# Optimization experiments

Measured on AMD Instinct MI355X. Metric: run time of the kernel, lower is better.

## Reference

```python
import jax, jax.numpy as jnp
import numpy as np

B, N, C, K = 4, 1024, 384, 10


def _sqdist(a, b):
    # a: [B,P,3], b: [B,M,3] -> [B,P,M] squared euclidean distance
    d = (jnp.sum(a * a, -1)[:, :, None] + jnp.sum(b * b, -1)[:, None, :]
         - 2.0 * jnp.einsum('bpc,bmc->bpm', a, b))
    return jnp.maximum(d, 0.0)


def _gather(points, idx):
    # points: [B,M,C], idx: [B,...] int -> [B,...,C]  (index_points)
    return jax.vmap(lambda p, i: p[i])(points, idx)


def setup_inputs() -> dict:
    key = jax.random.key(0)
    ks = jax.random.split(key, 8)
    def lin(k_, fan_in, fan_out):
        return jax.random.normal(k_, (fan_in, fan_out), jnp.float32) * (1.0 / np.sqrt(fan_in))
    return {
        'q': jax.random.normal(ks[0], (B, N, C), jnp.float32),
        'q_pos': jax.random.normal(ks[1], (B, N, 3), jnp.float32),
        'Wv': lin(ks[2], C, C), 'bv': jnp.zeros((C,), jnp.float32),
        'W1': lin(ks[3], 2 * C, C), 'b1': jnp.zeros((C,), jnp.float32),
        'ln_g': jnp.ones((C,), jnp.float32), 'ln_b': jnp.zeros((C,), jnp.float32),
        'W2': lin(ks[4], C, 3),
        'Wk': lin(ks[5], 2 * C, C), 'bk': jnp.zeros((C,), jnp.float32),
    }


def reference(q, q_pos, Wv, bv, W1, b1, ln_g, ln_b, W2, Wk, bk):
    Bq, Nq, Cq = q.shape
    # 1) KNN of each query among all points (self-attn: v=q, v_pos=q_pos)
    d = _sqdist(q_pos, q_pos)                      # [B,N,N]
    _, idx = jax.lax.top_k(-d, K)                  # [B,N,K] (smallest distances)
    # 2) offset prediction from gathered projected features + query feature
    v_off = q @ Wv + bv                            # [B,N,C]
    off_local_v = _gather(v_off, idx)              # [B,N,K,C]
    qk = jnp.broadcast_to(q[:, :, None, :], (Bq, Nq, K, Cq))
    shift_feat = jnp.concatenate([off_local_v, qk], -1)  # [B,N,K,2C]
    h = shift_feat @ W1 + b1
    mu = jnp.mean(h, -1, keepdims=True)
    var = jnp.var(h, -1, keepdims=True)
    h = (h - mu) / jnp.sqrt(var + 1e-5) * ln_g + ln_b     # LayerNorm
    h = jax.nn.gelu(h, approximate=False)
    offset = jnp.tanh(h @ W2)                      # [B,N,K,3]
    # 3) deformed positions, scaled by half the local bbox extent
    local_v_pos = _gather(q_pos, idx)              # [B,N,K,3]
    scale = (local_v_pos.max(-2) - local_v_pos.min(-2))[:, :, None, :] * 0.5
    shift_pos = (local_v_pos + offset * scale).reshape(Bq, Nq * K, 3)
    # 4) three_nn + three_interpolate (inverse-squared-distance weights)
    d2 = _sqdist(shift_pos, q_pos)                 # [B,NK,N]
    negd, idx3 = jax.lax.top_k(-d2, 3)             # [B,NK,3]
    dist = -negd
    w = 1.0 / (dist + 1e-8)
    w = w / jnp.sum(w, -1, keepdims=True)
    feats3 = _gather(q, idx3)                      # [B,NK,3,C]
    interp = jnp.einsum('bpt,bptc->bpc', w, feats3).reshape(Bq, Nq, K, Cq)
    # 5) graph conv: concat(diff, q) -> Linear -> LeakyReLU(0.2) -> max over K
    feature = jnp.concatenate([interp - qk, qk], -1)      # [B,N,K,2C]
    out = jax.nn.leaky_relu(feature @ Wk + bk, negative_slope=0.2)
    return out.max(-2)                             # [B,N,C]
```

## Files before the change

kernel.cpp:

```cpp
#include <hip/hip_runtime.h>
#include <math.h>

#define BB 4
#define NN 1024
#define CC 384
#define KK 10
#define NKK (NN*KK)

typedef __attribute__((ext_vector_type(8))) short short8v;
typedef __attribute__((ext_vector_type(8))) unsigned short ushort8v;
typedef __attribute__((ext_vector_type(4))) float f32x4;

template <int NA>
__device__ __forceinline__ void wave_sum_arr(float* a) {
  #pragma unroll
  for (int off = 32; off > 0; off >>= 1) {
    float t[NA];
    #pragma unroll
    for (int u = 0; u < NA; ++u) t[u] = __shfl_xor(a[u], off, 64);
    #pragma unroll
    for (int u = 0; u < NA; ++u) a[u] += t[u];
  }
}

__device__ __forceinline__ unsigned short f2bf(float x) {
  unsigned int b = __float_as_uint(x);
  return (unsigned short)((b + 0x7fffu + ((b >> 16) & 1u)) >> 16);
}
__device__ __forceinline__ float bf2f(unsigned short h) {
  return __uint_as_float(((unsigned int)h) << 16);
}

#define NB_CVT  (BB * NN * CC / 1024)
#define NB_PB   (2 * CC * CC / 256)
#define NB_PREP (NB_CVT + NB_PB + 3)
__global__ __launch_bounds__(256) void prep_gemm_kernel(
    const float* __restrict__ q,
    const float* __restrict__ W1, const float* __restrict__ b1,
    const float* __restrict__ bv, const float* __restrict__ bk,
    const float* __restrict__ Wk, const float* __restrict__ Wv,
    unsigned short* __restrict__ qh, unsigned short* __restrict__ ql,
    unsigned short* __restrict__ Wt,
    float* __restrict__ bias_uv, float* __restrict__ bias_pb,
    float* __restrict__ M1p) {
  int blk = blockIdx.x;
  int tid = threadIdx.x;
  if (blk < NB_CVT) {
    int i = (blk * 256 + tid) * 4;
    float4 v = *reinterpret_cast<const float4*>(q + i);
    float x[4] = {v.x, v.y, v.z, v.w};
    #pragma unroll
    for (int j = 0; j < 4; ++j) {
      unsigned short h = f2bf(x[j]);
      qh[i + j] = h;
      ql[i + j] = f2bf(x[j] - bf2f(h));
    }
    return;
  }
  if (blk < NB_CVT + NB_PB) {
    int idx = (blk - NB_CVT) * 256 + tid;
    int n = idx / CC, k = idx % CC;
    float v;
    if (n < CC) v = Wk[(size_t)k * CC + n];
    else        v = Wk[(size_t)CC * CC + k * CC + (n - CC)] - Wk[(size_t)k * CC + (n - CC)];
    Wt[(size_t)n * CC + k] = f2bf(v);
    return;
  }
  if (blk < NB_PREP) {
    int j = (blk - NB_CVT - NB_PB) * 256 + tid;
    if (j >= 2 * CC) return;
    if (j < CC) { bias_uv[j] = 0.f; bias_pb[j] = 0.f; }
    else {
      int c = j - CC;
      float s = b1[c];
      for (int i = 0; i < CC; ++i) s += bv[i] * W1[i * CC + c];
      bias_uv[j] = s;
      bias_pb[j] = bk[c];
    }
    return;
  }
  {
    int r = blk - NB_PREP;
    int bx = r % 3, by = (r / 3) % 3, bz = r / 9;
    __shared__ float As[16][132];
    __shared__ float Bs[16][128];
    int tx = tid & 15, ty = tid >> 4;
    int row0 = by * 128, col0 = bx * 128;
    int k0 = bz * 48;
    float acc[8][8] = {};
    int arow = tid >> 2, akc = (tid & 3) << 2;
    int brow = tid >> 5, bcol = (tid & 31) << 2;
    for (int kt = k0; kt < k0 + 48; kt += 16) {
      #pragma unroll
      for (int h = 0; h < 2; ++h) {
        int rr = arow + 64 * h;
        float4 av = *reinterpret_cast<const float4*>(Wv + (size_t)(row0 + rr) * CC + kt + akc);
        As[akc + 0][rr] = av.x; As[akc + 1][rr] = av.y;
        As[akc + 2][rr] = av.z; As[akc + 3][rr] = av.w;
      }
      #pragma unroll
      for (int h = 0; h < 2; ++h) {
        int rr = brow + 8 * h;
        float4 bv4 = *reinterpret_cast<const float4*>(W1 + (size_t)(kt + rr) * CC + col0 + bcol);
        *reinterpret_cast<float4*>(&Bs[rr][bcol]) = bv4;
      }
      __syncthreads();
      #pragma unroll
      for (int kk = 0; kk < 16; ++kk) {
        float4 a0 = *reinterpret_cast<const float4*>(&As[kk][ty << 2]);
        float4 a1 = *reinterpret_cast<const float4*>(&As[kk][64 + (ty << 2)]);
        float4 b0 = *reinterpret_cast<const float4*>(&Bs[kk][tx << 2]);
        float4 b1 = *reinterpret_cast<const float4*>(&Bs[kk][64 + (tx << 2)]);
        float av_[8] = {a0.x, a0.y, a0.z, a0.w, a1.x, a1.y, a1.z, a1.w};
        float bv_[8] = {b0.x, b0.y, b0.z, b0.w, b1.x, b1.y, b1.z, b1.w};
        #pragma unroll
        for (int i = 0; i < 8; ++i)
          #pragma unroll
          for (int j = 0; j < 8; ++j) acc[i][j] += av_[i] * bv_[j];
      }
      __syncthreads();
    }
    float* Cz = M1p + (size_t)bz * CC * CC;
    #pragma unroll
    for (int i = 0; i < 8; ++i) {
      int row = row0 + (ty << 2) + (i & 3) + ((i & 4) << 4);
      if (row >= CC) continue;
      #pragma unroll
      for (int h = 0; h < 2; ++h) {
        int col = col0 + 64 * h + (tx << 2);
        if (col >= CC) continue;
        float4 rv;
        rv.x = acc[i][4 * h + 0]; rv.y = acc[i][4 * h + 1];
        rv.z = acc[i][4 * h + 2]; rv.w = acc[i][4 * h + 3];
        *reinterpret_cast<float4*>(Cz + (size_t)row * CC + col) = rv;
      }
    }
  }
}

__global__ void pack_uv_split_kernel(const float* __restrict__ M1p, const float* __restrict__ W1,
                                     unsigned short* __restrict__ Buvh,
                                     unsigned short* __restrict__ Buvl) {
  int idx = blockIdx.x * 256 + threadIdx.x;
  int k = idx / (2 * CC), n = idx % (2 * CC);
  float val;
  if (n < CC) {
    float s = 0.f;
    #pragma unroll
    for (int p = 0; p < 8; ++p) s += M1p[(size_t)p * CC * CC + (size_t)k * CC + n];
    val = s;
  } else {
    val = W1[(size_t)(CC + k) * CC + (n - CC)];
  }
  unsigned short h = f2bf(val);
  Buvh[(size_t)n * CC + k] = h;
  Buvl[(size_t)n * CC + k] = f2bf(val - bf2f(h));
}

__global__ __launch_bounds__(256) void gemm_mfma_kernel(
    const unsigned short* __restrict__ qh, const unsigned short* __restrict__ ql,
    const unsigned short* __restrict__ Buvh, const unsigned short* __restrict__ Buvl,
    const unsigned short* __restrict__ Wt,
    float* __restrict__ Cuv, float* __restrict__ Cpb,
    const float* __restrict__ bias_uv, const float* __restrict__ bias_pb) {
  int path = blockIdx.z;
  const unsigned short* Bh = path ? Wt : Buvh;
  float* Cm = path ? Cpb : Cuv;
  const float* bias = path ? bias_pb : bias_uv;
  __shared__ unsigned short Ah[128 * 32], Alo[128 * 32];
  __shared__ unsigned short Bhs[128 * 32], Bls[128 * 32];
  int tid = threadIdx.x;
  int lane = tid & 63, w = tid >> 6;
  int m0 = blockIdx.y * 128, n0 = blockIdx.x * 128;
  f32x4 acc[4][4];
  #pragma unroll
  for (int i = 0; i < 4; ++i)
    #pragma unroll
    for (int j = 0; j < 4; ++j) acc[i][j] = (f32x4){0.f, 0.f, 0.f, 0.f};
  int rl = lane & 15, kg = lane >> 4;
  for (int k0 = 0; k0 < CC; k0 += 32) {
    #pragma unroll
    for (int j = 0; j < 2; ++j) {
      int id = tid + 256 * j;
      int r = id >> 2, s = id & 3;
      int sw = (s ^ (r & 3)) * 8;
      *reinterpret_cast<ushort8v*>(Ah + r * 32 + sw) =
          *reinterpret_cast<const ushort8v*>(qh + (size_t)(m0 + r) * CC + k0 + s * 8);
      *reinterpret_cast<ushort8v*>(Bhs + r * 32 + sw) =
          *reinterpret_cast<const ushort8v*>(Bh + (size_t)(n0 + r) * CC + k0 + s * 8);
      if (!path) {
        *reinterpret_cast<ushort8v*>(Alo + r * 32 + sw) =
            *reinterpret_cast<const ushort8v*>(ql + (size_t)(m0 + r) * CC + k0 + s * 8);
        *reinterpret_cast<ushort8v*>(Bls + r * 32 + sw) =
            *reinterpret_cast<const ushort8v*>(Buvl + (size_t)(n0 + r) * CC + k0 + s * 8);
      }
    }
    __syncthreads();
    short8v afh[4], bfh[4], afl[4], bfl[4];
    #pragma unroll
    for (int f = 0; f < 4; ++f) {
      int ar = (w & 1) * 64 + f * 16 + rl;
      int aof = ar * 32 + (kg ^ (ar & 3)) * 8;
      int br = (w >> 1) * 64 + f * 16 + rl;
      int bof = br * 32 + (kg ^ (br & 3)) * 8;
      afh[f] = *reinterpret_cast<const short8v*>(Ah + aof);
      bfh[f] = *reinterpret_cast<const short8v*>(Bhs + bof);
      if (!path) {
        afl[f] = *reinterpret_cast<const short8v*>(Alo + aof);
        bfl[f] = *reinterpret_cast<const short8v*>(Bls + bof);
      }
    }
    #pragma unroll
    for (int i = 0; i < 4; ++i) {
      #pragma unroll
      for (int j = 0; j < 4; ++j) {
        acc[i][j] = __builtin_amdgcn_mfma_f32_16x16x32_bf16(afh[i], bfh[j], acc[i][j], 0, 0, 0);
        if (!path) {
          acc[i][j] = __builtin_amdgcn_mfma_f32_16x16x32_bf16(afh[i], bfl[j], acc[i][j], 0, 0, 0);
          acc[i][j] = __builtin_amdgcn_mfma_f32_16x16x32_bf16(afl[i], bfh[j], acc[i][j], 0, 0, 0);
        }
      }
    }
    __syncthreads();
  }
  #pragma unroll
  for (int i = 0; i < 4; ++i) {
    #pragma unroll
    for (int j = 0; j < 4; ++j) {
      int col = n0 + (w >> 1) * 64 + j * 16 + rl;
      float bcol_v = bias[col];
      #pragma unroll
      for (int r = 0; r < 4; ++r) {
        int row = m0 + (w & 1) * 64 + i * 16 + kg * 4 + r;
        Cm[(size_t)row * (2 * CC) + col] = acc[i][j][r] + bcol_v;
      }
    }
  }
}

__global__ __launch_bounds__(256) void tail_kernel(
    const float* __restrict__ Cat_uv, const float* __restrict__ Cat_pb,
    const float* __restrict__ lng, const float* __restrict__ lnb,
    const float* __restrict__ W2, const float* __restrict__ q_pos,
    float* __restrict__ out) {
  int blk = blockIdx.x;
  int b = blk >> 8;
  int ng = blk & 255;
  int tid = threadIdx.x;
  int wave = tid >> 6, lane = tid & 63;
  int n = ng * 4 + wave;
  int bn = b * NN + n;
  __shared__ float4 sp4[NN];
  __shared__ int s_nb[4][KK];
  __shared__ float s_shp[4][KK][3];
  __shared__ float s_w[4][KK][3];
  __shared__ int s_i[4][KK][3];

  const float* qp = q_pos + (size_t)b * NN * 3;
  for (int i = tid; i < NN; i += 256) {
    float x = qp[i * 3 + 0], y = qp[i * 3 + 1], z = qp[i * 3 + 2];
    sp4[i] = (float4){x, y, z, x * x + y * y + z * z};
  }
  float Vv[6], lg[6], lb[6], w2a[6], w2b[6], w2c[6];
  const float* Vrow = Cat_uv + (size_t)bn * (2 * CC) + CC;
  #pragma unroll
  for (int i = 0; i < 6; ++i) {
    int c = lane + (i << 6);
    Vv[i] = Vrow[c];
    lg[i] = lng[c]; lb[i] = lnb[c];
    w2a[i] = W2[c * 3 + 0]; w2b[i] = W2[c * 3 + 1]; w2c[i] = W2[c * 3 + 2];
  }
  __syncthreads();

  {
    float4 me = sp4[n];
    float px = me.x, py = me.y, pz = me.z, sp = me.w;
    float bd[KK]; int bi[KK];
    #pragma unroll
    for (int s = 0; s < KK; ++s) { bd[s] = 1e30f; bi[s] = -1; }
    #pragma unroll 4
    for (int j = 0; j < 16; ++j) {
      int m = lane + (j << 6);
      float4 c = sp4[m];
      float dot = fmaf(px, c.x, fmaf(py, c.y, pz * c.z));
      float d = fmaf(-2.f, dot, sp + c.w);
      d = fmaxf(d, 0.f);
      if (d < bd[KK - 1]) {
        bd[KK - 1] = d; bi[KK - 1] = m;
        #pragma unroll
        for (int s = KK - 1; s >= 1; --s) {
          if (bd[s] < bd[s - 1]) {
            float td = bd[s]; bd[s] = bd[s - 1]; bd[s - 1] = td;
            int ti = bi[s]; bi[s] = bi[s - 1]; bi[s - 1] = ti;
          }
        }
      }
    }
    for (int s = 0; s < KK; ++s) {
      float d = bd[0]; int i = bi[0];
      #pragma unroll
      for (int off = 32; off > 0; off >>= 1) {
        float od = __shfl_xor(d, off, 64);
        int oi = __shfl_xor(i, off, 64);
        if (od < d || (od == d && oi < i)) { d = od; i = oi; }
      }
      if (bi[0] == i) {
        #pragma unroll
        for (int u = 0; u < KK - 1; ++u) { bd[u] = bd[u + 1]; bi[u] = bi[u + 1]; }
        bd[KK - 1] = 1e30f; bi[KK - 1] = -1;
      }
      if (lane == 0) s_nb[wave][s] = i;
    }
  }
  __syncthreads();

  int nb[KK];
  #pragma unroll
  for (int s = 0; s < KK; ++s) nb[s] = s_nb[wave][s];
  float sclx, scly, sclz;
  {
    float mxx = -1e30f, mnx = 1e30f, mxy = -1e30f, mny = 1e30f, mxz = -1e30f, mnz = 1e30f;
    #pragma unroll
    for (int k2 = 0; k2 < KK; ++k2) {
      float4 c = sp4[nb[k2]];
      mxx = fmaxf(mxx, c.x); mnx = fminf(mnx, c.x);
      mxy = fmaxf(mxy, c.y); mny = fminf(mny, c.y);
      mxz = fmaxf(mxz, c.z); mnz = fminf(mnz, c.z);
    }
    sclx = (mxx - mnx) * 0.5f; scly = (mxy - mny) * 0.5f; sclz = (mxz - mnz) * 0.5f;
  }

  #pragma unroll
  for (int half = 0; half < 2; ++half) {
    int kb = half * 5;
    float hk[5][6];
    float sum[5];
    #pragma unroll
    for (int kk = 0; kk < 5; ++kk) {
      const float* Urow = Cat_uv + ((size_t)b * NN + nb[kb + kk]) * (2 * CC);
      float s = 0.f;
      #pragma unroll
      for (int i = 0; i < 6; ++i) {
        hk[kk][i] = Urow[lane + (i << 6)] + Vv[i];
        s += hk[kk][i];
      }
      sum[kk] = s;
    }
    wave_sum_arr<5>(sum);
    float mu[5], var[5];
    #pragma unroll
    for (int kk = 0; kk < 5; ++kk) {
      mu[kk] = sum[kk] * (1.0f / CC);
      float v = 0.f;
      #pragma unroll
      for (int i = 0; i < 6; ++i) { float d = hk[kk][i] - mu[kk]; v += d * d; }
      var[kk] = v;
    }
    wave_sum_arr<5>(var);
    float o[15];
    #pragma unroll
    for (int kk = 0; kk < 5; ++kk) {
      float rstd = 1.0f / sqrtf(var[kk] * (1.0f / CC) + 1e-5f);
      float o0 = 0.f, o1 = 0.f, o2 = 0.f;
      #pragma unroll
      for (int i = 0; i < 6; ++i) {
        float x = (hk[kk][i] - mu[kk]) * rstd * lg[i] + lb[i];
        float g = 0.5f * x * (1.0f + erff(x * 0.70710678118654752440f));
        o0 = fmaf(g, w2a[i], o0); o1 = fmaf(g, w2b[i], o1); o2 = fmaf(g, w2c[i], o2);
      }
      o[kk * 3 + 0] = o0; o[kk * 3 + 1] = o1; o[kk * 3 + 2] = o2;
    }
    wave_sum_arr<15>(o);
    if (lane == 0) {
      #pragma unroll
      for (int kk = 0; kk < 5; ++kk) {
        int k = kb + kk;
        float4 lv = sp4[nb[k]];
        s_shp[wave][k][0] = lv.x + tanhf(o[kk * 3 + 0]) * sclx;
        s_shp[wave][k][1] = lv.y + tanhf(o[kk * 3 + 1]) * scly;
        s_shp[wave][k][2] = lv.z + tanhf(o[kk * 3 + 2]) * sclz;
      }
    }
  }
  __syncthreads();

  #pragma unroll
  for (int p = 0; p < KK; ++p) {
    float px = s_shp[wave][p][0], py = s_shp[wave][p][1], pz = s_shp[wave][p][2];
    float sp = fmaf(px, px, fmaf(py, py, pz * pz));
    float d0 = 1e30f, d1 = 1e30f, d2 = 1e30f;
    int i0 = -1, i1 = -1, i2 = -1;
    #pragma unroll 4
    for (int j = 0; j < 16; ++j) {
      int m = lane + (j << 6);
      float4 c = sp4[m];
      float dot = fmaf(px, c.x, fmaf(py, c.y, pz * c.z));
      float d = fmaf(-2.f, dot, sp + c.w);
      d = fmaxf(d, 0.f);
      bool c2 = d < d2, c1 = d < d1, c0 = d < d0;
      d2 = c1 ? d1 : (c2 ? d : d2);  i2 = c1 ? i1 : (c2 ? m : i2);
      d1 = c0 ? d0 : (c1 ? d : d1);  i1 = c0 ? i0 : (c1 ? m : i1);
      d0 = c0 ? d : d0;              i0 = c0 ? m : i0;
    }
    float wd[3]; int wi[3];
    #pragma unroll
    for (int s = 0; s < 3; ++s) {
      float d = d0; int i = i0;
      #pragma unroll
      for (int off = 32; off > 0; off >>= 1) {
        float od = __shfl_xor(d, off, 64);
        int oi = __shfl_xor(i, off, 64);
        if (od < d || (od == d && oi < i)) { d = od; i = oi; }
      }
      if (i0 == i) { d0 = d1; i0 = i1; d1 = d2; i1 = i2; d2 = 1e30f; i2 = -1; }
      wd[s] = d; wi[s] = i;
    }
    if (lane == 0) {
      float w0 = 1.f / (wd[0] + 1e-8f), w1 = 1.f / (wd[1] + 1e-8f), w2 = 1.f / (wd[2] + 1e-8f);
      float s = w0 + w1 + w2;
      s_w[wave][p][0] = w0 / s; s_w[wave][p][1] = w1 / s; s_w[wave][p][2] = w2 / s;
      s_i[wave][p][0] = wi[0];  s_i[wave][p][1] = wi[1];  s_i[wave][p][2] = wi[2];
    }
  }
  __syncthreads();

  const float* Pb = Cat_pb + (size_t)b * NN * (2 * CC);
  const float* BseRow = Cat_pb + (size_t)bn * (2 * CC) + CC;
  #pragma unroll 2
  for (int ci = 0; ci < 6; ++ci) {
    int c = lane + (ci << 6);
    float base = BseRow[c];
    float best = -1e30f;
    #pragma unroll
    for (int k = 0; k < KK; ++k) {
      float acc = base;
      #pragma unroll
      for (int tt = 0; tt < 3; ++tt)
        acc = fmaf(s_w[wave][k][tt], Pb[(size_t)s_i[wave][k][tt] * (2 * CC) + c], acc);
      acc = acc >= 0.f ? acc : 0.2f * acc;
      best = fmaxf(best, acc);
    }
    out[(size_t)bn * CC + c] = best;
  }
}

extern "C" void kernel_launch(void* const* d_in, const int* in_sizes, int n_in,
                              void* d_out, int out_size, void* d_ws, size_t ws_size,
                              hipStream_t stream) {
  (void)in_sizes; (void)n_in; (void)out_size; (void)ws_size;
  const float* q    = (const float*)d_in[0];
  const float* qpos = (const float*)d_in[1];
  const float* Wv   = (const float*)d_in[2];
  const float* bv   = (const float*)d_in[3];
  const float* W1   = (const float*)d_in[4];
  const float* b1   = (const float*)d_in[5];
  const float* lng  = (const float*)d_in[6];
  const float* lnb  = (const float*)d_in[7];
  const float* W2   = (const float*)d_in[8];
  const float* Wk   = (const float*)d_in[9];
  const float* bk   = (const float*)d_in[10];
  float* out = (float*)d_out;

  float* ws = (float*)d_ws;
  float* Cat_uv = ws; ws += (size_t)BB * NN * 2 * CC;
  float* Cat_pb = ws; ws += (size_t)BB * NN * 2 * CC;
  float* M1p = Cat_pb;
  float* bias_uv = ws; ws += 2 * CC;
  float* bias_pb = ws; ws += 2 * CC;
  unsigned short* qh = (unsigned short*)ws;  ws += (size_t)BB * NN * CC / 2;
  unsigned short* ql = (unsigned short*)ws;  ws += (size_t)BB * NN * CC / 2;
  unsigned short* Wt = (unsigned short*)ws;  ws += (size_t)2 * CC * CC / 2;
  unsigned short* Buvh = (unsigned short*)ws; ws += (size_t)2 * CC * CC / 2;
  unsigned short* Buvl = (unsigned short*)ws; ws += (size_t)2 * CC * CC / 2;

  prep_gemm_kernel<<<dim3(NB_PREP + 72), dim3(256), 0, stream>>>(
      q, W1, b1, bv, bk, Wk, Wv, qh, ql, Wt, bias_uv, bias_pb, M1p);
  pack_uv_split_kernel<<<dim3(CC * 2 * CC / 256), dim3(256), 0, stream>>>(M1p, W1, Buvh, Buvl);
  gemm_mfma_kernel<<<dim3(2 * CC / 128, BB * NN / 128, 2), dim3(256), 0, stream>>>(
      qh, ql, Buvh, Buvl, Wt, Cat_uv, Cat_pb, bias_uv, bias_pb);
  tail_kernel<<<dim3(BB * NN / 4), dim3(256), 0, stream>>>(
      Cat_uv, Cat_pb, lng, lnb, W2, qpos, out);
}
```

Baseline: 171.6 us.

## Split tail kernel into geometry and per-query interpolation kernels

Splits the fused tail kernel in two. The first computes KNN, the offset MLP and the shifted positions, writing them to a workspace buffer. The second runs one block per query, spreading the 10 three-NN searches over 4 waves and the final gather/max over all 256 threads. This removes a block-wide sync and a serial per-wave loop over the ten shifted points, giving more parallelism in the interpolation stage. The cost is an extra launch, a global round trip for the shifted positions, and each of the 4096 interp blocks rebuilding the 1024-point position table in shared memory.

```diff
diff --git a/kernel.cpp b/kernel.cpp
--- a/kernel.cpp
+++ b/kernel.cpp
@@ -238,11 +238,10 @@
   }
 }
 
-__global__ __launch_bounds__(256) void tail_kernel(
-    const float* __restrict__ Cat_uv, const float* __restrict__ Cat_pb,
-    const float* __restrict__ lng, const float* __restrict__ lnb,
+__global__ __launch_bounds__(256) void geo_kernel(
+    const float* __restrict__ Cat_uv, const float* __restrict__ lng, const float* __restrict__ lnb,
     const float* __restrict__ W2, const float* __restrict__ q_pos,
-    float* __restrict__ out) {
+    float* __restrict__ shp) {
   int blk = blockIdx.x;
   int b = blk >> 8;
   int ng = blk & 255;
@@ -251,10 +250,6 @@
   int n = ng * 4 + wave;
   int bn = b * NN + n;
   __shared__ float4 sp4[NN];
-  __shared__ int s_nb[4][KK];
-  __shared__ float s_shp[4][KK][3];
-  __shared__ float s_w[4][KK][3];
-  __shared__ int s_i[4][KK][3];
 
   const float* qp = q_pos + (size_t)b * NN * 3;
   for (int i = tid; i < NN; i += 256) {
@@ -272,6 +267,7 @@
   }
   __syncthreads();
 
+  int nb[KK];
   {
     float4 me = sp4[n];
     float px = me.x, py = me.y, pz = me.z, sp = me.w;
@@ -296,6 +292,7 @@
         }
       }
     }
+    #pragma unroll
     for (int s = 0; s < KK; ++s) {
       float d = bd[0]; int i = bi[0];
       #pragma unroll
@@ -309,14 +306,10 @@
         for (int u = 0; u < KK - 1; ++u) { bd[u] = bd[u + 1]; bi[u] = bi[u + 1]; }
         bd[KK - 1] = 1e30f; bi[KK - 1] = -1;
       }
-      if (lane == 0) s_nb[wave][s] = i;
-    }
-  }
-  __syncthreads();
-
-  int nb[KK];
-  #pragma unroll
-  for (int s = 0; s < KK; ++s) nb[s] = s_nb[wave][s];
+      nb[s] = i;
+    }
+  }
+
   float sclx, scly, sclz;
   {
     float mxx = -1e30f, mnx = 1e30f, mxy = -1e30f, mny = 1e30f, mxz = -1e30f, mnz = 1e30f;
@@ -330,6 +323,7 @@
     sclx = (mxx - mnx) * 0.5f; scly = (mxy - mny) * 0.5f; sclz = (mxz - mnz) * 0.5f;
   }
 
+  float ox = 0.f, oy = 0.f, oz = 0.f;
   #pragma unroll
   for (int half = 0; half < 2; ++half) {
     int kb = half * 5;
@@ -371,64 +365,110 @@
       o[kk * 3 + 0] = o0; o[kk * 3 + 1] = o1; o[kk * 3 + 2] = o2;
     }
     wave_sum_arr<15>(o);
-    if (lane == 0) {
-      #pragma unroll
-      for (int kk = 0; kk < 5; ++kk) {
-        int k = kb + kk;
-        float4 lv = sp4[nb[k]];
-        s_shp[wave][k][0] = lv.x + tanhf(o[kk * 3 + 0]) * sclx;
-        s_shp[wave][k][1] = lv.y + tanhf(o[kk * 3 + 1]) * scly;
-        s_shp[wave][k][2] = lv.z + tanhf(o[kk * 3 + 2]) * sclz;
-      }
-    }
-  }
+    #pragma unroll
+    for (int kk = 0; kk < 5; ++kk) {
+      if (lane == kb + kk) { ox = o[kk * 3 + 0]; oy = o[kk * 3 + 1]; oz = o[kk * 3 + 2]; }
+    }
+  }
+  int myn = 0;
+  #pragma unroll
+  for (int k = 0; k < KK; ++k) if (lane == k) myn = nb[k];
+  if (lane < KK) {
+    float4 lv = sp4[myn];
+    float* sp = shp + ((size_t)bn * KK + lane) * 3;
+    sp[0] = lv.x + tanhf(ox) * sclx;
+    sp[1] = lv.y + tanhf(oy) * scly;
+    sp[2] = lv.z + tanhf(oz) * sclz;
+  }
+}
+
+__global__ __launch_bounds__(256) void interp_kernel(
+    const float* __restrict__ Cat_pb, const float* __restrict__ q_pos,
+    const float* __restrict__ shp, float* __restrict__ out) {
+  int bn = blockIdx.x;
+  int b = bn >> 10;
+  int tid = threadIdx.x;
+  int wave = tid >> 6, lane = tid & 63;
+  __shared__ float4 sp4[NN];
+  __shared__ float s_shp[KK * 3];
+  __shared__ float s_w[KK][3];
+  __shared__ int s_i[KK][3];
+
+  const float* qp = q_pos + (size_t)b * NN * 3;
+  for (int i = tid; i < NN; i += 256) {
+    float x = qp[i * 3 + 0], y = qp[i * 3 + 1], z = qp[i * 3 + 2];
+    sp4[i] = (float4){x, y, z, x * x + y * y + z * z};
+  }
+  if (tid < KK * 3) s_shp[tid] = shp[(size_t)bn * KK * 3 + tid];
   __syncthreads();
 
-  #pragma unroll
-  for (int p = 0; p < KK; ++p) {
-    float px = s_shp[wave][p][0], py = s_shp[wave][p][1], pz = s_shp[wave][p][2];
-    float sp = fmaf(px, px, fmaf(py, py, pz * pz));
-    float d0 = 1e30f, d1 = 1e30f, d2 = 1e30f;
-    int i0 = -1, i1 = -1, i2 = -1;
-    #pragma unroll 4
-    for (int j = 0; j < 16; ++j) {
-      int m = lane + (j << 6);
-      float4 c = sp4[m];
-      float dot = fmaf(px, c.x, fmaf(py, c.y, pz * c.z));
-      float d = fmaf(-2.f, dot, sp + c.w);
+  int cnt = (wave < 2) ? 3 : 2;
+  int pbase = (wave < 2) ? wave * 3 : 6 + (wave - 2) * 2;
+  float px[3], py[3], pz[3], ps[3];
+  #pragma unroll
+  for (int j = 0; j < 3; ++j) {
+    int p = pbase + (j < cnt ? j : cnt - 1);
+    px[j] = s_shp[p * 3 + 0]; py[j] = s_shp[p * 3 + 1]; pz[j] = s_shp[p * 3 + 2];
+    ps[j] = fmaf(px[j], px[j], fmaf(py[j], py[j], pz[j] * pz[j]));
+  }
+  float d0[3], d1[3], d2[3]; int i0[3], i1[3], i2[3];
+  #pragma unroll
+  for (int j = 0; j < 3; ++j) { d0[j] = d1[j] = d2[j] = 1e30f; i0[j] = i1[j] = i2[j] = -1; }
+  #pragma unroll 4
+  for (int it = 0; it < 16; ++it) {
+    int m = lane + (it << 6);
+    float4 c = sp4[m];
+    #pragma unroll
+    for (int j = 0; j < 3; ++j) {
+      float dot = fmaf(px[j], c.x, fmaf(py[j], c.y, pz[j] * c.z));
+      float d = fmaf(-2.f, dot, ps[j] + c.w);
       d = fmaxf(d, 0.f);
-      bool c2 = d < d2, c1 = d < d1, c0 = d < d0;
-      d2 = c1 ? d1 : (c2 ? d : d2);  i2 = c1 ? i1 : (c2 ? m : i2);
-      d1 = c0 ? d0 : (c1 ? d : d1);  i1 = c0 ? i0 : (c1 ? m : i1);
-      d0 = c0 ? d : d0;              i0 = c0 ? m : i0;
-    }
-    float wd[3]; int wi[3];
-    #pragma unroll
-    for (int s = 0; s < 3; ++s) {
-      float d = d0; int i = i0;
-      #pragma unroll
-      for (int off = 32; off > 0; off >>= 1) {
-        float od = __shfl_xor(d, off, 64);
-        int oi = __shfl_xor(i, off, 64);
-        if (od < d || (od == d && oi < i)) { d = od; i = oi; }
-      }
-      if (i0 == i) { d0 = d1; i0 = i1; d1 = d2; i1 = i2; d2 = 1e30f; i2 = -1; }
-      wd[s] = d; wi[s] = i;
-    }
-    if (lane == 0) {
-      float w0 = 1.f / (wd[0] + 1e-8f), w1 = 1.f / (wd[1] + 1e-8f), w2 = 1.f / (wd[2] + 1e-8f);
-      float s = w0 + w1 + w2;
-      s_w[wave][p][0] = w0 / s; s_w[wave][p][1] = w1 / s; s_w[wave][p][2] = w2 / s;
-      s_i[wave][p][0] = wi[0];  s_i[wave][p][1] = wi[1];  s_i[wave][p][2] = wi[2];
+      bool c2 = d < d2[j], c1 = d < d1[j], c0 = d < d0[j];
+      d2[j] = c1 ? d1[j] : (c2 ? d : d2[j]);  i2[j] = c1 ? i1[j] : (c2 ? m : i2[j]);
+      d1[j] = c0 ? d0[j] : (c1 ? d : d1[j]);  i1[j] = c0 ? i0[j] : (c1 ? m : i1[j]);
+      d0[j] = c0 ? d : d0[j];                 i0[j] = c0 ? m : i0[j];
+    }
+  }
+  float wd[3][3]; int wi[3][3];
+  #pragma unroll
+  for (int s = 0; s < 3; ++s) {
+    float d[3]; int ii[3];
+    #pragma unroll
+    for (int j = 0; j < 3; ++j) { d[j] = d0[j]; ii[j] = i0[j]; }
+    #pragma unroll
+    for (int off = 32; off > 0; off >>= 1) {
+      #pragma unroll
+      for (int j = 0; j < 3; ++j) {
+        float od = __shfl_xor(d[j], off, 64);
+        int oi = __shfl_xor(ii[j], off, 64);
+        if (od < d[j] || (od == d[j] && oi < ii[j])) { d[j] = od; ii[j] = oi; }
+      }
+    }
+    #pragma unroll
+    for (int j = 0; j < 3; ++j) {
+      if (i0[j] == ii[j]) {
+        d0[j] = d1[j]; i0[j] = i1[j]; d1[j] = d2[j]; i1[j] = i2[j]; d2[j] = 1e30f; i2[j] = -1;
+      }
+      wd[s][j] = d[j]; wi[s][j] = ii[j];
+    }
+  }
+  if (lane == 0) {
+    #pragma unroll
+    for (int j = 0; j < 3; ++j) {
+      if (j < cnt) {
+        float w0 = 1.f / (wd[0][j] + 1e-8f), w1 = 1.f / (wd[1][j] + 1e-8f), w2 = 1.f / (wd[2][j] + 1e-8f);
+        float s = w0 + w1 + w2;
+        int p = pbase + j;
+        s_w[p][0] = w0 / s; s_w[p][1] = w1 / s; s_w[p][2] = w2 / s;
+        s_i[p][0] = wi[0][j]; s_i[p][1] = wi[1][j]; s_i[p][2] = wi[2][j];
+      }
     }
   }
   __syncthreads();
 
   const float* Pb = Cat_pb + (size_t)b * NN * (2 * CC);
   const float* BseRow = Cat_pb + (size_t)bn * (2 * CC) + CC;
-  #pragma unroll 2
-  for (int ci = 0; ci < 6; ++ci) {
-    int c = lane + (ci << 6);
+  for (int c = tid; c < CC; c += 256) {
     float base = BseRow[c];
     float best = -1e30f;
     #pragma unroll
@@ -436,7 +476,7 @@
       float acc = base;
       #pragma unroll
       for (int tt = 0; tt < 3; ++tt)
-        acc = fmaf(s_w[wave][k][tt], Pb[(size_t)s_i[wave][k][tt] * (2 * CC) + c], acc);
+        acc = fmaf(s_w[k][tt], Pb[(size_t)s_i[k][tt] * (2 * CC) + c], acc);
       acc = acc >= 0.f ? acc : 0.2f * acc;
       best = fmaxf(best, acc);
     }
@@ -467,6 +507,7 @@
   float* M1p = Cat_pb;
   float* bias_uv = ws; ws += 2 * CC;
   float* bias_pb = ws; ws += 2 * CC;
+  float* shp = ws; ws += (size_t)BB * NKK * 3;
   unsigned short* qh = (unsigned short*)ws;  ws += (size_t)BB * NN * CC / 2;
   unsigned short* ql = (unsigned short*)ws;  ws += (size_t)BB * NN * CC / 2;
   unsigned short* Wt = (unsigned short*)ws;  ws += (size_t)2 * CC * CC / 2;
@@ -478,6 +519,8 @@
   pack_uv_split_kernel<<<dim3(CC * 2 * CC / 256), dim3(256), 0, stream>>>(M1p, W1, Buvh, Buvl);
   gemm_mfma_kernel<<<dim3(2 * CC / 128, BB * NN / 128, 2), dim3(256), 0, stream>>>(
       qh, ql, Buvh, Buvl, Wt, Cat_uv, Cat_pb, bias_uv, bias_pb);
-  tail_kernel<<<dim3(BB * NN / 4), dim3(256), 0, stream>>>(
-      Cat_uv, Cat_pb, lng, lnb, W2, qpos, out);
-}
+  geo_kernel<<<dim3(BB * NN / 4), dim3(256), 0, stream>>>(
+      Cat_uv, lng, lnb, W2, qpos, shp);
+  interp_kernel<<<dim3(BB * NN), dim3(256), 0, stream>>>(
+      Cat_pb, qpos, shp, out);
+}
```

Result: faster. 161.2 us (-6.1%).
